# Performance work log

Hardware: AMD Instinct MI355X
Metric: run time of the kernel (lower is better)

The kernel has to match this reference:

```python
import jax, jax.numpy as jnp
import numpy as np

DIM = 1024
N_HEADS = 16
HEAD_DIM = DIM // N_HEADS


def setup_inputs() -> dict:
    key = jax.random.key(0)
    k_x, k_qkv, k_out = jax.random.split(key, 3)
    B, L = 4, 2048
    x = jax.random.normal(k_x, (B, L, DIM), dtype=jnp.float32)
    # torch Linear weight has shape [out, in]; y = x @ W.T
    s = 1.0 / np.sqrt(DIM)
    W_qkv = jax.random.uniform(k_qkv, (3 * DIM, DIM), dtype=jnp.float32, minval=-s, maxval=s)
    W_out = jax.random.uniform(k_out, (DIM, DIM), dtype=jnp.float32, minval=-s, maxval=s)
    return {"x": x, "W_qkv": W_qkv, "W_out": W_out}


def reference(x, W_qkv, W_out):
    B, L, D = x.shape
    H, Hd = N_HEADS, HEAD_DIM
    scale = Hd ** (-0.5)
    qkv = x @ W_qkv.T                       # [B, L, 3D]
    q, k, v = jnp.split(qkv, 3, axis=-1)
    # 'b l (h d) -> b h l d'
    q = q.reshape(B, L, H, Hd).transpose(0, 2, 1, 3)
    k = k.reshape(B, L, H, Hd).transpose(0, 2, 1, 3)
    v = v.reshape(B, L, H, Hd).transpose(0, 2, 1, 3)
    attn = jnp.einsum('bhld,bhmd->bhlm', q, k) * scale  # [B, H, L, L]
    causal = jnp.tril(jnp.ones((L, L), dtype=bool))
    attn = jnp.where(causal, attn, -jnp.inf)
    attn = jax.nn.softmax(attn, axis=-1)
    out = jnp.einsum('bhlm,bhmd->bhld', attn, v)        # [B, H, L, Hd]
    out = out.transpose(0, 2, 1, 3).reshape(B, L, D)    # 'b h l d -> b l (h d)'
    return out @ W_out.T
```

## Files before the change

kernel.cpp:

```cpp
#include <hip/hip_runtime.h>
#include <stdint.h>

#define BATCH 4
#define SEQ   2048
#define DIM_  1024
#define NHEAD 16
#define HDIM  64

#define QSC 0.18033688011112042f

typedef __attribute__((ext_vector_type(8)))  short bf8;
typedef __attribute__((ext_vector_type(4)))  short s4v;
typedef __attribute__((ext_vector_type(4)))  float f4;
typedef __attribute__((ext_vector_type(16))) float f16v;
typedef __attribute__((ext_vector_type(2)))  unsigned int u2;
typedef __attribute__((ext_vector_type(4)))  unsigned int u4;

#define MFMA(a, b, c)   __builtin_amdgcn_mfma_f32_16x16x32_bf16(a, b, c, 0, 0, 0)
#define MFMA32(a, b, c) __builtin_amdgcn_mfma_f32_32x32x16_bf16(a, b, c, 0, 0, 0)

#define BAR_LGKM() asm volatile("s_waitcnt lgkmcnt(0)\n\ts_barrier" ::: "memory")
#define PBAR() asm volatile("s_barrier" ::: "memory")

static __device__ __forceinline__ short f2b(float f) {
    uint32_t u = __builtin_bit_cast(uint32_t, f);
    u = (u + 0x7FFFu + ((u >> 16) & 1u)) >> 16;
    return (short)u;
}

static __device__ __forceinline__ uint32_t cvtpk(float lo, float hi) {
    uint32_t r;
    asm("v_cvt_pk_bf16_f32 %0, %1, %2" : "=v"(r) : "v"(lo), "v"(hi));
    return r;
}

typedef const uint32_t __attribute__((address_space(1)))* gas_t;
typedef uint32_t __attribute__((address_space(3)))* las_t;
static __device__ __forceinline__ void gl_lds16(const short* g, short* l) {
    __builtin_amdgcn_global_load_lds((gas_t)g, (las_t)l, 16, 0, 0);
}

__global__ void cvt_all(const float* __restrict__ x, const float* __restrict__ wq,
                        const float* __restrict__ wo, short* __restrict__ xb,
                        short* __restrict__ wqb, short* __restrict__ wob) {
    const int NX = BATCH * SEQ * DIM_ / 4, NQ = 3 * DIM_ * DIM_ / 4;
    int i = blockIdx.x * blockDim.x + threadIdx.x;
    const float4* in; s4v* out; int j;
    if (i < NX)           { in = (const float4*)x;  out = (s4v*)xb;  j = i; }
    else if (i < NX + NQ) { in = (const float4*)wq; out = (s4v*)wqb; j = i - NX; }
    else                  { in = (const float4*)wo; out = (s4v*)wob; j = i - NX - NQ; }
    float4 v = in[j];
    s4v o;
    o.x = f2b(v.x); o.y = f2b(v.y); o.z = f2b(v.z); o.w = f2b(v.w);
    out[j] = o;
}

#define LDSB 24576
#define NT   16

#define PG_PROLOG()                                                           \
    __shared__ __align__(16) short lds[3 * LDSB];                             \
    const int tid  = threadIdx.x;                                             \
    const int lane = tid & 63;                                                \
    const int wave = tid >> 6;                                                \
    const int quad = lane >> 4, l16 = lane & 15;                              \
    const int wr = wave >> 1, wc = wave & 1;                                  \
    const int m0 = blockIdx.y * 256;                                          \
    const int n0 = blockIdx.x * 128;                                          \
    \
    const short* gA[4]; int dA[4];                                            \
    _Pragma("unroll") for (int j = 0; j < 4; ++j) {                           \
        const int idx = j * 512 + tid;                                        \
        const int row = idx >> 3, pos = idx & 7;                              \
        gA[j] = A + (size_t)(m0 + row) * 1024 + (pos ^ (row & 7)) * 8;        \
        dA[j] = idx * 8;                                                      \
    }                                                                         \
    const short* gB[2]; int dB[2];                                            \
    _Pragma("unroll") for (int j = 0; j < 2; ++j) {                           \
        const int idx = j * 512 + tid;                                        \
        const int row = idx >> 3, pos = idx & 7;                              \
        gB[j] = W + (size_t)(n0 + row) * 1024 + (pos ^ (row & 7)) * 8;        \
        dB[j] = 16384 + idx * 8;                                              \
    }                                                                         \
                       \
    int aro[4], bro[4];                                                       \
    _Pragma("unroll") for (int i = 0; i < 4; ++i) {                           \
        aro[i] = (wr * 64 + i * 16 + l16) * 64;                               \
        bro[i] = 16384 + (wc * 64 + i * 16 + l16) * 64;                       \
    }                                                                         \
    const int kx = l16 & 7;                                                   \
    short* cur = lds; short* nxt = lds + LDSB; short* stg = lds + 2 * LDSB;   \
    f4 acc[4][4] = {};

#define PG_STAGE6(bp)                                                         \
    do {                                                                      \
        gl_lds16(gA[0], (bp) + dA[0]); gl_lds16(gA[1], (bp) + dA[1]);         \
        gl_lds16(gA[2], (bp) + dA[2]); gl_lds16(gA[3], (bp) + dA[3]);         \
        gl_lds16(gB[0], (bp) + dB[0]); gl_lds16(gB[1], (bp) + dB[1]);         \
        _Pragma("unroll") for (int j = 0; j < 4; ++j) gA[j] += 64;            \
        gB[0] += 64; gB[1] += 64;                                             \
    } while (0)

#define PG_KLOOP()                                                            \
    PG_STAGE6(cur);                                               \
    PG_STAGE6(nxt);                                               \
    asm volatile("s_waitcnt vmcnt(6)\n\ts_barrier" ::: "memory");             \
    for (int t = 0; t < NT; ++t) {                                            \
        const bool pre = (t < NT - 2);                                        \
        bf8 a[4], b[4];                                                       \
                                              \
        _Pragma("unroll") for (int i = 0; i < 4; ++i) {                       \
            a[i] = *(const bf8*)(cur + aro[i] + ((0 + quad) ^ kx) * 8);       \
            b[i] = *(const bf8*)(cur + bro[i] + ((0 + quad) ^ kx) * 8);       \
        }                                                                     \
        if (pre) {                                                            \
            gl_lds16(gA[0], stg + dA[0]); gl_lds16(gA[1], stg + dA[1]);       \
            gl_lds16(gA[2], stg + dA[2]);                                     \
        }                                                                     \
        PBAR();                                                               \
        __builtin_amdgcn_s_setprio(1);                                        \
        _Pragma("unroll") for (int mt = 0; mt < 4; ++mt)                      \
            _Pragma("unroll") for (int nt = 0; nt < 4; ++nt)                  \
                acc[mt][nt] = MFMA(a[mt], b[nt], acc[mt][nt]);                \
        __builtin_amdgcn_s_setprio(0);                                        \
        PBAR();                                                               \
                                              \
        _Pragma("unroll") for (int i = 0; i < 4; ++i) {                       \
            a[i] = *(const bf8*)(cur + aro[i] + ((4 + quad) ^ kx) * 8);       \
            b[i] = *(const bf8*)(cur + bro[i] + ((4 + quad) ^ kx) * 8);       \
        }                                                                     \
        if (pre) {                                                            \
            gl_lds16(gA[3], stg + dA[3]);                                     \
            gl_lds16(gB[0], stg + dB[0]); gl_lds16(gB[1], stg + dB[1]);       \
            _Pragma("unroll") for (int j = 0; j < 4; ++j) gA[j] += 64;        \
            gB[0] += 64; gB[1] += 64;                                         \
        }                                                                     \
        PBAR();                                                               \
        __builtin_amdgcn_s_setprio(1);                                        \
        _Pragma("unroll") for (int mt = 0; mt < 4; ++mt)                      \
            _Pragma("unroll") for (int nt = 0; nt < 4; ++nt)                  \
                acc[mt][nt] = MFMA(a[mt], b[nt], acc[mt][nt]);                \
        __builtin_amdgcn_s_setprio(0);                                        \
         \
        if (pre) asm volatile("s_waitcnt vmcnt(6)\n\ts_barrier" ::: "memory");\
        else     asm volatile("s_waitcnt vmcnt(0)\n\ts_barrier" ::: "memory");\
        short* tmp = cur; cur = nxt; nxt = stg; stg = tmp;                    \
    }

__global__ __launch_bounds__(512, 2) void gemm_qkv(const short* __restrict__ A,
                                                   const short* __restrict__ W,
                                                   short* __restrict__ Qd,
                                                   short* __restrict__ Kd,
                                                   short* __restrict__ Vd) {
    PG_PROLOG();
    PG_KLOOP();

    short* const bases[3] = {Qd, Kd, Vd};
    #pragma unroll
    for (int mt = 0; mt < 4; ++mt) {
        const int row = m0 + wr * 64 + mt * 16 + quad * 4;
        #pragma unroll
        for (int nt = 0; nt < 4; ++nt) {
            const int colb  = n0 + wc * 64 + nt * 16;
            const int which = colb >> 10;
            const int hh    = (colb >> 6) & 15;
            const int d0    = colb & 63;
            const float sc_ = (which == 0) ? QSC : 1.0f;
            short* bp = bases[which];
            #pragma unroll
            for (int r = 0; r < 4; ++r) {
                const int t  = row + r;
                const int bb = t >> 11, ll = t & 2047;
                bp[((size_t)(bb * NHEAD + hh) * SEQ + ll) * 64 + d0 + l16] =
                    f2b(acc[mt][nt][r] * sc_);
            }
        }
    }
}

__global__ __launch_bounds__(512, 2) void gemm_bt(const short* __restrict__ A,
                                                  const short* __restrict__ W,
                                                  float* __restrict__ Cp) {
    PG_PROLOG();
    PG_KLOOP();

    #pragma unroll
    for (int mt = 0; mt < 4; ++mt) {
        const int row = m0 + wr * 64 + mt * 16 + quad * 4;
        #pragma unroll
        for (int nt = 0; nt < 4; ++nt) {
            const int col = n0 + wc * 64 + nt * 16 + l16;
            #pragma unroll
            for (int r = 0; r < 4; ++r)
                Cp[(size_t)(row + r) * DIM_ + col] = acc[mt][nt][r];
        }
    }
}

__global__ __launch_bounds__(256) void flash_attn(const short* __restrict__ Qd,
                                                  const short* __restrict__ Kd,
                                                  const short* __restrict__ Vd,
                                                  short* __restrict__ out) {
    const int bh = blockIdx.x;
    const int b  = bh >> 4, h = bh & 15;
    const int qt = (gridDim.y - 1) - blockIdx.y;
    const int q0 = qt * 128;
    const int tid  = threadIdx.x;
    const int lane = tid & 63, wave = tid >> 6;
    const int l32  = lane & 31, khalf = lane >> 5;

    __shared__ __align__(16) short Ks[64 * 72];
    __shared__ __align__(16) short Vt[64 * 72];
    uint32_t* Vt32 = (uint32_t*)Vt;

    const short* Qp = Qd + (size_t)bh * (SEQ * 64);
    const short* Kp = Kd + (size_t)bh * (SEQ * 64);
    const short* Vp = Vd + (size_t)bh * (SEQ * 64);

    const int qrow = q0 + wave * 32 + l32;
    bf8 qf[4];
    #pragma unroll
    for (int dk = 0; dk < 4; ++dk)
        qf[dk] = *(const bf8*)(Qp + (size_t)qrow * 64 + dk * 16 + khalf * 8);

    const int skey = tid >> 2, sc = tid & 3;
    const int vkp = tid & 31, vds = (tid >> 5) * 8;

    bf8 ka0 = *(const bf8*)(Kp + (size_t)skey * 64 + sc * 8);
    bf8 ka1 = *(const bf8*)(Kp + (size_t)skey * 64 + (sc + 4) * 8);
    bf8 vr0 = *(const bf8*)(Vp + (size_t)(2 * vkp) * 64 + vds);
    bf8 vr1 = *(const bf8*)(Vp + (size_t)(2 * vkp + 1) * 64 + vds);

    f16v o0 = {}, o1 = {};
    float lsum = 0.f;
    const bf8 zz = {};

    const int nIter = 2 * qt + 2;
    for (int it = 0; it < nIter; ++it) {
        const int k0 = it * 64;

        BAR_LGKM();
        *(bf8*)(&Ks[skey * 72 + sc * 8])       = ka0;
        *(bf8*)(&Ks[skey * 72 + (sc + 4) * 8]) = ka1;
        #pragma unroll
        for (int i = 0; i < 8; ++i) {
            uint32_t p = (uint32_t)(uint16_t)vr0[i] | ((uint32_t)(uint16_t)vr1[i] << 16);
            Vt32[(vds + i) * 36 + vkp] = p;
        }
        BAR_LGKM();

        if (it + 1 < nIter) {
            const int kn = k0 + 64;
            ka0 = *(const bf8*)(Kp + (size_t)(kn + skey) * 64 + sc * 8);
            ka1 = *(const bf8*)(Kp + (size_t)(kn + skey) * 64 + (sc + 4) * 8);
            vr0 = *(const bf8*)(Vp + (size_t)(kn + 2 * vkp) * 64 + vds);
            vr1 = *(const bf8*)(Vp + (size_t)(kn + 2 * vkp + 1) * 64 + vds);
        }

        if (q0 + wave * 32 < k0) continue;

        bf8 pf[4];
        #pragma unroll
        for (int kt = 0; kt < 2; ++kt) {
            const int ktbase = k0 + kt * 32;
            const int rel = (q0 + wave * 32) - ktbase;
            if (rel < 0) {
                pf[kt * 2] = zz; pf[kt * 2 + 1] = zz;
                continue;
            }
            f16v st = {};
            __builtin_amdgcn_s_setprio(1);
            #pragma unroll
            for (int dk = 0; dk < 4; ++dk) {
                bf8 kf = *(const bf8*)(&Ks[(kt * 32 + l32) * 72 + dk * 16 + khalf * 8]);
                st = MFMA32(kf, qf[dk], st);
            }
            __builtin_amdgcn_s_setprio(0);
            float P[16];
            if (rel == 0) {
                #pragma unroll
                for (int r = 0; r < 16; ++r) {
                    const int kg = ktbase + (r & 3) + 8 * (r >> 2) + 4 * khalf;
                    float pv = __builtin_amdgcn_exp2f(st[r]);
                    P[r] = (kg > qrow) ? 0.0f : pv;
                }
            } else {
                #pragma unroll
                for (int r = 0; r < 16; ++r) P[r] = __builtin_amdgcn_exp2f(st[r]);
            }
            uint32_t w0 = cvtpk(P[0],  P[1]),  w1 = cvtpk(P[2],  P[3]);
            uint32_t w2 = cvtpk(P[4],  P[5]),  w3 = cvtpk(P[6],  P[7]);
            uint32_t w4 = cvtpk(P[8],  P[9]),  w5 = cvtpk(P[10], P[11]);
            uint32_t w6 = cvtpk(P[12], P[13]), w7 = cvtpk(P[14], P[15]);
            u2 s02 = __builtin_amdgcn_permlane32_swap(w0, w2, false, false);
            u2 s13 = __builtin_amdgcn_permlane32_swap(w1, w3, false, false);
            u2 s46 = __builtin_amdgcn_permlane32_swap(w4, w6, false, false);
            u2 s57 = __builtin_amdgcn_permlane32_swap(w5, w7, false, false);
            u4 q0w = {s02[0], s13[0], s02[1], s13[1]};
            u4 q1w = {s46[0], s57[0], s46[1], s57[1]};
            pf[kt * 2]     = __builtin_bit_cast(bf8, q0w);
            pf[kt * 2 + 1] = __builtin_bit_cast(bf8, q1w);
            float ls = ((P[0] + P[1]) + (P[2] + P[3])) +
                       ((P[4] + P[5]) + (P[6] + P[7])) +
                       ((P[8] + P[9]) + (P[10] + P[11])) +
                       ((P[12] + P[13]) + (P[14] + P[15]));
            lsum += ls;
        }

        __builtin_amdgcn_s_setprio(1);
        #pragma unroll
        for (int ks = 0; ks < 4; ++ks) {
            bf8 v0 = *(const bf8*)(&Vt[(l32) * 72 + ks * 16 + khalf * 8]);
            bf8 v1 = *(const bf8*)(&Vt[(32 + l32) * 72 + ks * 16 + khalf * 8]);
            o0 = MFMA32(pf[ks], v0, o0);
            o1 = MFMA32(pf[ks], v1, o1);
        }
        __builtin_amdgcn_s_setprio(0);
    }

    lsum += __shfl_xor(lsum, 32);
    short* outp = out + ((size_t)(b * SEQ + q0 + wave * 32) * DIM_) + h * 64;
    #pragma unroll
    for (int r = 0; r < 16; ++r) {
        const int rowl = (r & 3) + 8 * (r >> 2) + 4 * khalf;
        const float inv = 1.0f / __shfl(lsum, rowl);
        outp[(size_t)rowl * DIM_ + l32]      = f2b(o0[r] * inv);
        outp[(size_t)rowl * DIM_ + 32 + l32] = f2b(o1[r] * inv);
    }
}

extern "C" void kernel_launch(void* const* d_in, const int* in_sizes, int n_in,
                              void* d_out, int out_size, void* d_ws, size_t ws_size,
                              hipStream_t stream) {
    const float* x    = (const float*)d_in[0];
    const float* wqkv = (const float*)d_in[1];
    const float* wout = (const float*)d_in[2];

    char* ws = (char*)d_ws;
    short* xb    = (short*)(ws);
    short* wqkvb = (short*)(ws + (size_t)(16) * (1 << 20));
    short* woutb = (short*)(ws + (size_t)(22) * (1 << 20));
    short* Qd    = (short*)(ws + (size_t)(24) * (1 << 20));
    short* Kd    = (short*)(ws + (size_t)(40) * (1 << 20));
    short* Vd    = (short*)(ws + (size_t)(56) * (1 << 20));
    short* attnb = (short*)(ws + (size_t)(72) * (1 << 20));

    const int ntot = (BATCH * SEQ * DIM_ + 3 * DIM_ * DIM_ + DIM_ * DIM_) / 4;
    cvt_all<<<(ntot + 255) / 256, 256, 0, stream>>>(x, wqkv, wout, xb, wqkvb, woutb);

    gemm_qkv<<<dim3(3 * DIM_ / 128, BATCH * SEQ / 256), 512, 0, stream>>>(
        xb, wqkvb, Qd, Kd, Vd);

    flash_attn<<<dim3(BATCH * NHEAD, SEQ / 128), 256, 0, stream>>>(Qd, Kd, Vd, attnb);

    gemm_bt<<<dim3(DIM_ / 128, BATCH * SEQ / 256), 512, 0, stream>>>(
        attnb, woutb, (float*)d_out);
}
```

Baseline: 232.4 us.

## Enlarge GEMM tiles to 256x256 with double-buffered LDS and swizzled block order

Both projection GEMMs move from 256x128 tiles with triple-buffered LDS to 256x256 tiles with two LDS buffers. Each wave now computes a 128x64 sub-tile, and the k-loop is split into four MFMA phases with finer-grained global-to-LDS prefetch and waits. Workgroup IDs are remapped by a modular swizzle to improve L2 reuse across neighbouring blocks. The larger tile raises arithmetic intensity but doubles accumulator registers (128 floats per thread) and halves grid size (384 and 128 blocks), which can cost occupancy or leave CUs idle on the output GEMM.

Measured after the change: 235.8 us. About the same (+1.5%).

```diff
diff --git a/kernel.cpp b/kernel.cpp
--- a/kernel.cpp
+++ b/kernel.cpp
@@ -55,96 +55,101 @@
     out[j] = o;
 }
 
-#define LDSB 24576
-#define NT   16
+#define NT 16
 
 #define PG_PROLOG()                                                           \
-    __shared__ __align__(16) short lds[3 * LDSB];                             \
+    __shared__ __align__(16) short lds[2 * 32768];                            \
     const int tid  = threadIdx.x;                                             \
     const int lane = tid & 63;                                                \
     const int wave = tid >> 6;                                                \
     const int quad = lane >> 4, l16 = lane & 15;                              \
-    const int wr = wave >> 1, wc = wave & 1;                                  \
-    const int m0 = blockIdx.y * 256;                                          \
-    const int n0 = blockIdx.x * 128;                                          \
-    \
-    const short* gA[4]; int dA[4];                                            \
+    const int wr = wave >> 2, wc = wave & 3;                                  \
+                     \
+    const int gx  = gridDim.x;                                                \
+    const int nwg = gx * gridDim.y;                                           \
+    const int lid = blockIdx.y * gx + blockIdx.x;                             \
+    const int swz = (lid & 7) * (nwg >> 3) + (lid >> 3);                      \
+    const int m0 = (swz / gx) * 256;                                          \
+    const int n0 = (swz % gx) * 256;                                          \
+    const short* gA[4]; const short* gB[4]; int dA[4];                        \
     _Pragma("unroll") for (int j = 0; j < 4; ++j) {                           \
         const int idx = j * 512 + tid;                                        \
         const int row = idx >> 3, pos = idx & 7;                              \
         gA[j] = A + (size_t)(m0 + row) * 1024 + (pos ^ (row & 7)) * 8;        \
+        gB[j] = W + (size_t)(n0 + row) * 1024 + (pos ^ (row & 7)) * 8;        \
         dA[j] = idx * 8;                                                      \
     }                                                                         \
-    const short* gB[2]; int dB[2];                                            \
-    _Pragma("unroll") for (int j = 0; j < 2; ++j) {                           \
-        const int idx = j * 512 + tid;                                        \
-        const int row = idx >> 3, pos = idx & 7;                              \
-        gB[j] = W + (size_t)(n0 + row) * 1024 + (pos ^ (row & 7)) * 8;        \
-        dB[j] = 16384 + idx * 8;                                              \
-    }                                                                         \
-                       \
-    int aro[4], bro[4];                                                       \
-    _Pragma("unroll") for (int i = 0; i < 4; ++i) {                           \
-        aro[i] = (wr * 64 + i * 16 + l16) * 64;                               \
-        bro[i] = 16384 + (wc * 64 + i * 16 + l16) * 64;                       \
-    }                                                                         \
-    const int kx = l16 & 7;                                                   \
-    short* cur = lds; short* nxt = lds + LDSB; short* stg = lds + 2 * LDSB;   \
-    f4 acc[4][4] = {};
-
-#define PG_STAGE6(bp)                                                         \
-    do {                                                                      \
-        gl_lds16(gA[0], (bp) + dA[0]); gl_lds16(gA[1], (bp) + dA[1]);         \
-        gl_lds16(gA[2], (bp) + dA[2]); gl_lds16(gA[3], (bp) + dA[3]);         \
-        gl_lds16(gB[0], (bp) + dB[0]); gl_lds16(gB[1], (bp) + dB[1]);         \
-        _Pragma("unroll") for (int j = 0; j < 4; ++j) gA[j] += 64;            \
-        gB[0] += 64; gB[1] += 64;                                             \
-    } while (0)
+    int aoff[8], boff[4];                                                     \
+    _Pragma("unroll") for (int i = 0; i < 8; ++i)                             \
+        aoff[i] = (wr * 128 + i * 16 + l16) * 64;                             \
+    _Pragma("unroll") for (int i = 0; i < 4; ++i)                             \
+        boff[i] = 16384 + (wc * 64 + i * 16 + l16) * 64;                      \
+    const int kx  = l16 & 7;                                                  \
+    const int kc0 = ((0 + quad) ^ kx) * 8;                                    \
+    const int kc1 = ((4 + quad) ^ kx) * 8;                                    \
+    short* cur = lds; short* nxt = lds + 32768;                               \
+    f4 acc[8][4] = {};
+
+#define PG_ISSUE_B01(bp) do { gl_lds16(gB[0], (bp) + 16384 + dA[0]);          \
+                              gl_lds16(gB[1], (bp) + 16384 + dA[1]); } while (0)
+#define PG_ISSUE_B23(bp) do { gl_lds16(gB[2], (bp) + 16384 + dA[2]);          \
+                              gl_lds16(gB[3], (bp) + 16384 + dA[3]); } while (0)
+#define PG_ISSUE_A(bp)   do { gl_lds16(gA[0], (bp) + dA[0]);                  \
+                              gl_lds16(gA[2], (bp) + dA[2]);                  \
+                              gl_lds16(gA[1], (bp) + dA[1]);                  \
+                              gl_lds16(gA[3], (bp) + dA[3]); } while (0)
+#define PG_BUMP() _Pragma("unroll") for (int j = 0; j < 4; ++j) { gA[j] += 64; gB[j] += 64; }
+
+#define PG_MFMA16(ACCB, AV)                                                   \
+    __builtin_amdgcn_s_setprio(1);                                            \
+    _Pragma("unroll") for (int mt = 0; mt < 4; ++mt)                          \
+        _Pragma("unroll") for (int nt = 0; nt < 4; ++nt)                      \
+            acc[ACCB + mt][nt] = MFMA(AV[mt], b[nt], acc[ACCB + mt][nt]);     \
+    __builtin_amdgcn_s_setprio(0);
 
 #define PG_KLOOP()                                                            \
-    PG_STAGE6(cur);                                               \
-    PG_STAGE6(nxt);                                               \
-    asm volatile("s_waitcnt vmcnt(6)\n\ts_barrier" ::: "memory");             \
+    PG_ISSUE_B01(cur); PG_ISSUE_B23(cur); PG_ISSUE_A(cur);                    \
+    PG_BUMP();                                                                \
+    asm volatile("s_waitcnt vmcnt(2)\n\ts_barrier" ::: "memory");             \
     for (int t = 0; t < NT; ++t) {                                            \
-        const bool pre = (t < NT - 2);                                        \
+        const bool pre = (t < NT - 1);                                        \
         bf8 a[4], b[4];                                                       \
-                                              \
+                                                \
         _Pragma("unroll") for (int i = 0; i < 4; ++i) {                       \
-            a[i] = *(const bf8*)(cur + aro[i] + ((0 + quad) ^ kx) * 8);       \
-            b[i] = *(const bf8*)(cur + bro[i] + ((0 + quad) ^ kx) * 8);       \
+            a[i] = *(const bf8*)(cur + aoff[i] + kc0);                        \
+            b[i] = *(const bf8*)(cur + boff[i] + kc0);                        \
         }                                                                     \
-        if (pre) {                                                            \
-            gl_lds16(gA[0], stg + dA[0]); gl_lds16(gA[1], stg + dA[1]);       \
-            gl_lds16(gA[2], stg + dA[2]);                                     \
+        if (pre) PG_ISSUE_B01(nxt);                                           \
+        PBAR();                                                               \
+        PG_MFMA16(0, a);                                                      \
+                     \
+        if (pre) asm volatile("s_waitcnt vmcnt(2)\n\ts_barrier" ::: "memory");\
+        else     asm volatile("s_waitcnt vmcnt(0)\n\ts_barrier" ::: "memory");\
+                                     \
+        bf8 a2[4];                                                            \
+        _Pragma("unroll") for (int i = 0; i < 4; ++i)                         \
+            a2[i] = *(const bf8*)(cur + aoff[4 + i] + kc0);                   \
+        if (pre) PG_ISSUE_B23(nxt);                                           \
+        PBAR();                                                               \
+        PG_MFMA16(4, a2);                                                     \
+        PBAR();                                                               \
+                                                \
+        _Pragma("unroll") for (int i = 0; i < 4; ++i) {                       \
+            a[i] = *(const bf8*)(cur + aoff[i] + kc1);                        \
+            b[i] = *(const bf8*)(cur + boff[i] + kc1);                        \
         }                                                                     \
-        PBAR();                                                               \
-        __builtin_amdgcn_s_setprio(1);                                        \
-        _Pragma("unroll") for (int mt = 0; mt < 4; ++mt)                      \
-            _Pragma("unroll") for (int nt = 0; nt < 4; ++nt)                  \
-                acc[mt][nt] = MFMA(a[mt], b[nt], acc[mt][nt]);                \
-        __builtin_amdgcn_s_setprio(0);                                        \
-        PBAR();                                                               \
-                                              \
-        _Pragma("unroll") for (int i = 0; i < 4; ++i) {                       \
-            a[i] = *(const bf8*)(cur + aro[i] + ((4 + quad) ^ kx) * 8);       \
-            b[i] = *(const bf8*)(cur + bro[i] + ((4 + quad) ^ kx) * 8);       \
-        }                                                                     \
-        if (pre) {                                                            \
-            gl_lds16(gA[3], stg + dA[3]);                                     \
-            gl_lds16(gB[0], stg + dB[0]); gl_lds16(gB[1], stg + dB[1]);       \
-            _Pragma("unroll") for (int j = 0; j < 4; ++j) gA[j] += 64;        \
-            gB[0] += 64; gB[1] += 64;                                         \
-        }                                                                     \
-        PBAR();                                                               \
-        __builtin_amdgcn_s_setprio(1);                                        \
-        _Pragma("unroll") for (int mt = 0; mt < 4; ++mt)                      \
-            _Pragma("unroll") for (int nt = 0; nt < 4; ++nt)                  \
-                acc[mt][nt] = MFMA(a[mt], b[nt], acc[mt][nt]);                \
-        __builtin_amdgcn_s_setprio(0);                                        \
-         \
-        if (pre) asm volatile("s_waitcnt vmcnt(6)\n\ts_barrier" ::: "memory");\
-        else     asm volatile("s_waitcnt vmcnt(0)\n\ts_barrier" ::: "memory");\
-        short* tmp = cur; cur = nxt; nxt = stg; stg = tmp;                    \
+        if (pre) { PG_ISSUE_A(nxt); PG_BUMP(); }                              \
+        PBAR();                                                               \
+        PG_MFMA16(0, a);                                                      \
+        PBAR();                                                               \
+                                                \
+        _Pragma("unroll") for (int i = 0; i < 4; ++i)                         \
+            a2[i] = *(const bf8*)(cur + aoff[4 + i] + kc1);                   \
+        PBAR();                                                               \
+        PG_MFMA16(4, a2);                                                     \
+               \
+        if (pre) asm volatile("s_waitcnt vmcnt(2)\n\ts_barrier" ::: "memory");\
+        short* tmp = cur; cur = nxt; nxt = tmp;                               \
     }
 
 __global__ __launch_bounds__(512, 2) void gemm_qkv(const short* __restrict__ A,
@@ -157,11 +162,11 @@
 
     short* const bases[3] = {Qd, Kd, Vd};
     #pragma unroll
-    for (int mt = 0; mt < 4; ++mt) {
-        const int row = m0 + wr * 64 + mt * 16 + quad * 4;
-        #pragma unroll
-        for (int nt = 0; nt < 4; ++nt) {
-            const int colb  = n0 + wc * 64 + nt * 16;
+    for (int mf = 0; mf < 8; ++mf) {
+        const int row = m0 + wr * 128 + mf * 16 + quad * 4;
+        #pragma unroll
+        for (int nf = 0; nf < 4; ++nf) {
+            const int colb  = n0 + wc * 64 + nf * 16;
             const int which = colb >> 10;
             const int hh    = (colb >> 6) & 15;
             const int d0    = colb & 63;
@@ -169,10 +174,10 @@
             short* bp = bases[which];
             #pragma unroll
             for (int r = 0; r < 4; ++r) {
-                const int t  = row + r;
-                const int bb = t >> 11, ll = t & 2047;
+                const int tk = row + r;
+                const int bb = tk >> 11, ll = tk & 2047;
                 bp[((size_t)(bb * NHEAD + hh) * SEQ + ll) * 64 + d0 + l16] =
-                    f2b(acc[mt][nt][r] * sc_);
+                    f2b(acc[mf][nf][r] * sc_);
             }
         }
     }
@@ -185,14 +190,14 @@
     PG_KLOOP();
 
     #pragma unroll
-    for (int mt = 0; mt < 4; ++mt) {
-        const int row = m0 + wr * 64 + mt * 16 + quad * 4;
-        #pragma unroll
-        for (int nt = 0; nt < 4; ++nt) {
-            const int col = n0 + wc * 64 + nt * 16 + l16;
+    for (int mf = 0; mf < 8; ++mf) {
+        const int row = m0 + wr * 128 + mf * 16 + quad * 4;
+        #pragma unroll
+        for (int nf = 0; nf < 4; ++nf) {
+            const int col = n0 + wc * 64 + nf * 16 + l16;
             #pragma unroll
             for (int r = 0; r < 4; ++r)
-                Cp[(size_t)(row + r) * DIM_ + col] = acc[mt][nt][r];
+                Cp[(size_t)(row + r) * DIM_ + col] = acc[mf][nf][r];
         }
     }
 }
@@ -348,11 +353,11 @@
     const int ntot = (BATCH * SEQ * DIM_ + 3 * DIM_ * DIM_ + DIM_ * DIM_) / 4;
     cvt_all<<<(ntot + 255) / 256, 256, 0, stream>>>(x, wqkv, wout, xb, wqkvb, woutb);
 
-    gemm_qkv<<<dim3(3 * DIM_ / 128, BATCH * SEQ / 256), 512, 0, stream>>>(
+    gemm_qkv<<<dim3(3 * DIM_ / 256, BATCH * SEQ / 256), 512, 0, stream>>>(
         xb, wqkvb, Qd, Kd, Vd);
 
     flash_attn<<<dim3(BATCH * NHEAD, SEQ / 128), 256, 0, stream>>>(Qd, Kd, Vd, attnb);
 
-    gemm_bt<<<dim3(DIM_ / 128, BATCH * SEQ / 256), 512, 0, stream>>>(
+    gemm_bt<<<dim3(DIM_ / 256, BATCH * SEQ / 256), 512, 0, stream>>>(
         attnb, woutb, (float*)d_out);
 }
```

## Pair causal query tiles per block, double-buffer K/V LDS, swizzle GEMM block order

Applied to the files above, without the earlier changes.

The flash-attention grid is halved so each block handles two query tiles, one long (15-y) and one short (y). This evens out the causal workload per block and removes the tail imbalance. K/V LDS tiles are now double-buffered, alternating by iteration parity. The GEMM prologue remaps block IDs with an XCD-style swizzle (lid&7 spread) so neighbouring tiles share L2. The risks are fewer blocks for occupancy, extra LDS per block, and a serial second tile that could lengthen per-block latency.

New measurement: 248.3 us. +6.9%, slower.

```diff
diff --git a/kernel.cpp b/kernel.cpp
--- a/kernel.cpp
+++ b/kernel.cpp
@@ -20,7 +20,6 @@
 #define MFMA32(a, b, c) __builtin_amdgcn_mfma_f32_32x32x16_bf16(a, b, c, 0, 0, 0)
 
 #define BAR_LGKM() asm volatile("s_waitcnt lgkmcnt(0)\n\ts_barrier" ::: "memory")
-#define PBAR() asm volatile("s_barrier" ::: "memory")
 
 static __device__ __forceinline__ short f2b(float f) {
     uint32_t u = __builtin_bit_cast(uint32_t, f);
@@ -58,6 +57,8 @@
 #define LDSB 24576
 #define NT   16
 
+#define PBAR() asm volatile("s_barrier" ::: "memory")
+
 #define PG_PROLOG()                                                           \
     __shared__ __align__(16) short lds[3 * LDSB];                             \
     const int tid  = threadIdx.x;                                             \
@@ -65,8 +66,12 @@
     const int wave = tid >> 6;                                                \
     const int quad = lane >> 4, l16 = lane & 15;                              \
     const int wr = wave >> 1, wc = wave & 1;                                  \
-    const int m0 = blockIdx.y * 256;                                          \
-    const int n0 = blockIdx.x * 128;                                          \
+    const int gx  = gridDim.x;                                                \
+    const int nwg = gx * gridDim.y;                                           \
+    const int lid = blockIdx.y * gx + blockIdx.x;                             \
+    const int swz = (lid & 7) * (nwg >> 3) + (lid >> 3);                      \
+    const int m0 = (swz / gx) * 256;                                          \
+    const int n0 = (swz % gx) * 128;                                          \
     \
     const short* gA[4]; int dA[4];                                            \
     _Pragma("unroll") for (int j = 0; j < 4; ++j) {                           \
@@ -203,129 +208,139 @@
                                                   short* __restrict__ out) {
     const int bh = blockIdx.x;
     const int b  = bh >> 4, h = bh & 15;
-    const int qt = (gridDim.y - 1) - blockIdx.y;
-    const int q0 = qt * 128;
     const int tid  = threadIdx.x;
     const int lane = tid & 63, wave = tid >> 6;
     const int l32  = lane & 31, khalf = lane >> 5;
 
-    __shared__ __align__(16) short Ks[64 * 72];
-    __shared__ __align__(16) short Vt[64 * 72];
-    uint32_t* Vt32 = (uint32_t*)Vt;
+    __shared__ __align__(16) short Ks[2][64 * 72];
+    __shared__ __align__(16) short Vt[2][64 * 72];
 
     const short* Qp = Qd + (size_t)bh * (SEQ * 64);
     const short* Kp = Kd + (size_t)bh * (SEQ * 64);
     const short* Vp = Vd + (size_t)bh * (SEQ * 64);
 
-    const int qrow = q0 + wave * 32 + l32;
-    bf8 qf[4];
-    #pragma unroll
-    for (int dk = 0; dk < 4; ++dk)
-        qf[dk] = *(const bf8*)(Qp + (size_t)qrow * 64 + dk * 16 + khalf * 8);
-
     const int skey = tid >> 2, sc = tid & 3;
     const int vkp = tid & 31, vds = (tid >> 5) * 8;
 
-    bf8 ka0 = *(const bf8*)(Kp + (size_t)skey * 64 + sc * 8);
-    bf8 ka1 = *(const bf8*)(Kp + (size_t)skey * 64 + (sc + 4) * 8);
-    bf8 vr0 = *(const bf8*)(Vp + (size_t)(2 * vkp) * 64 + vds);
-    bf8 vr1 = *(const bf8*)(Vp + (size_t)(2 * vkp + 1) * 64 + vds);
-
-    f16v o0 = {}, o1 = {};
-    float lsum = 0.f;
     const bf8 zz = {};
 
-    const int nIter = 2 * qt + 2;
-    for (int it = 0; it < nIter; ++it) {
-        const int k0 = it * 64;
-
-        BAR_LGKM();
-        *(bf8*)(&Ks[skey * 72 + sc * 8])       = ka0;
-        *(bf8*)(&Ks[skey * 72 + (sc + 4) * 8]) = ka1;
+    #pragma unroll 1
+    for (int half = 0; half < 2; ++half) {
+        const int qt = half ? blockIdx.y : (15 - blockIdx.y);
+        const int q0 = qt * 128;
+
+        const int qrow = q0 + wave * 32 + l32;
+        bf8 qf[4];
         #pragma unroll
-        for (int i = 0; i < 8; ++i) {
-            uint32_t p = (uint32_t)(uint16_t)vr0[i] | ((uint32_t)(uint16_t)vr1[i] << 16);
-            Vt32[(vds + i) * 36 + vkp] = p;
+        for (int dk = 0; dk < 4; ++dk)
+            qf[dk] = *(const bf8*)(Qp + (size_t)qrow * 64 + dk * 16 + khalf * 8);
+
+        bf8 ka0 = *(const bf8*)(Kp + (size_t)skey * 64 + sc * 8);
+        bf8 ka1 = *(const bf8*)(Kp + (size_t)skey * 64 + (sc + 4) * 8);
+        bf8 vr0 = *(const bf8*)(Vp + (size_t)(2 * vkp) * 64 + vds);
+        bf8 vr1 = *(const bf8*)(Vp + (size_t)(2 * vkp + 1) * 64 + vds);
+
+        f16v o0 = {}, o1 = {};
+        float lsum = 0.f;
+
+        const int nIter = 2 * qt + 2;
+        for (int it = 0; it < nIter; ++it) {
+            const int k0 = it * 64;
+            const int pb = it & 1;
+            short* Kb = Ks[pb];
+            short* Vb = Vt[pb];
+            uint32_t* Vb32 = (uint32_t*)Vb;
+
+            BAR_LGKM();
+            *(bf8*)(&Kb[skey * 72 + sc * 8])       = ka0;
+            *(bf8*)(&Kb[skey * 72 + (sc + 4) * 8]) = ka1;
+            #pragma unroll
+            for (int i = 0; i < 8; ++i) {
+                uint32_t p = (uint32_t)(uint16_t)vr0[i] |
+                             ((uint32_t)(uint16_t)vr1[i] << 16);
+                Vb32[(vds + i) * 36 + vkp] = p;
+            }
+            BAR_LGKM();
+
+            if (it + 1 < nIter) {
+                const int kn = k0 + 64;
+                ka0 = *(const bf8*)(Kp + (size_t)(kn + skey) * 64 + sc * 8);
+                ka1 = *(const bf8*)(Kp + (size_t)(kn + skey) * 64 + (sc + 4) * 8);
+                vr0 = *(const bf8*)(Vp + (size_t)(kn + 2 * vkp) * 64 + vds);
+                vr1 = *(const bf8*)(Vp + (size_t)(kn + 2 * vkp + 1) * 64 + vds);
+            }
+
+            if (q0 + wave * 32 < k0) continue;
+
+            bf8 pf[4];
+            #pragma unroll
+            for (int kt = 0; kt < 2; ++kt) {
+                const int ktbase = k0 + kt * 32;
+                const int rel = (q0 + wave * 32) - ktbase;
+                if (rel < 0) {
+                    pf[kt * 2] = zz; pf[kt * 2 + 1] = zz;
+                    continue;
+                }
+                f16v st = {};
+                __builtin_amdgcn_s_setprio(1);
+                #pragma unroll
+                for (int dk = 0; dk < 4; ++dk) {
+                    bf8 kf = *(const bf8*)(&Kb[(kt * 32 + l32) * 72 +
+                                               dk * 16 + khalf * 8]);
+                    st = MFMA32(kf, qf[dk], st);
+                }
+                __builtin_amdgcn_s_setprio(0);
+                float P[16];
+                if (rel == 0) {
+                    #pragma unroll
+                    for (int r = 0; r < 16; ++r) {
+                        const int kg = ktbase + (r & 3) + 8 * (r >> 2) + 4 * khalf;
+                        float pv = __builtin_amdgcn_exp2f(st[r]);
+                        P[r] = (kg > qrow) ? 0.0f : pv;
+                    }
+                } else {
+                    #pragma unroll
+                    for (int r = 0; r < 16; ++r) P[r] = __builtin_amdgcn_exp2f(st[r]);
+                }
+                uint32_t w0 = cvtpk(P[0],  P[1]),  w1 = cvtpk(P[2],  P[3]);
+                uint32_t w2 = cvtpk(P[4],  P[5]),  w3 = cvtpk(P[6],  P[7]);
+                uint32_t w4 = cvtpk(P[8],  P[9]),  w5 = cvtpk(P[10], P[11]);
+                uint32_t w6 = cvtpk(P[12], P[13]), w7 = cvtpk(P[14], P[15]);
+                u2 s02 = __builtin_amdgcn_permlane32_swap(w0, w2, false, false);
+                u2 s13 = __builtin_amdgcn_permlane32_swap(w1, w3, false, false);
+                u2 s46 = __builtin_amdgcn_permlane32_swap(w4, w6, false, false);
+                u2 s57 = __builtin_amdgcn_permlane32_swap(w5, w7, false, false);
+                u4 q0w = {s02[0], s13[0], s02[1], s13[1]};
+                u4 q1w = {s46[0], s57[0], s46[1], s57[1]};
+                pf[kt * 2]     = __builtin_bit_cast(bf8, q0w);
+                pf[kt * 2 + 1] = __builtin_bit_cast(bf8, q1w);
+                float ls = ((P[0] + P[1]) + (P[2] + P[3])) +
+                           ((P[4] + P[5]) + (P[6] + P[7])) +
+                           ((P[8] + P[9]) + (P[10] + P[11])) +
+                           ((P[12] + P[13]) + (P[14] + P[15]));
+                lsum += ls;
+            }
+
+            __builtin_amdgcn_s_setprio(1);
+            #pragma unroll
+            for (int ks = 0; ks < 4; ++ks) {
+                bf8 v0 = *(const bf8*)(&Vb[(l32) * 72 + ks * 16 + khalf * 8]);
+                bf8 v1 = *(const bf8*)(&Vb[(32 + l32) * 72 + ks * 16 + khalf * 8]);
+                o0 = MFMA32(pf[ks], v0, o0);
+                o1 = MFMA32(pf[ks], v1, o1);
+            }
+            __builtin_amdgcn_s_setprio(0);
         }
-        BAR_LGKM();
-
-        if (it + 1 < nIter) {
-            const int kn = k0 + 64;
-            ka0 = *(const bf8*)(Kp + (size_t)(kn + skey) * 64 + sc * 8);
-            ka1 = *(const bf8*)(Kp + (size_t)(kn + skey) * 64 + (sc + 4) * 8);
-            vr0 = *(const bf8*)(Vp + (size_t)(kn + 2 * vkp) * 64 + vds);
-            vr1 = *(const bf8*)(Vp + (size_t)(kn + 2 * vkp + 1) * 64 + vds);
+
+        lsum += __shfl_xor(lsum, 32);
+        short* outp = out + ((size_t)(b * SEQ + q0 + wave * 32) * DIM_) + h * 64;
+        #pragma unroll
+        for (int r = 0; r < 16; ++r) {
+            const int rowl = (r & 3) + 8 * (r >> 2) + 4 * khalf;
+            const float inv = 1.0f / __shfl(lsum, rowl);
+            outp[(size_t)rowl * DIM_ + l32]      = f2b(o0[r] * inv);
+            outp[(size_t)rowl * DIM_ + 32 + l32] = f2b(o1[r] * inv);
         }
-
-        if (q0 + wave * 32 < k0) continue;
-
-        bf8 pf[4];
-        #pragma unroll
-        for (int kt = 0; kt < 2; ++kt) {
-            const int ktbase = k0 + kt * 32;
-            const int rel = (q0 + wave * 32) - ktbase;
-            if (rel < 0) {
-                pf[kt * 2] = zz; pf[kt * 2 + 1] = zz;
-                continue;
-            }
-            f16v st = {};
-            __builtin_amdgcn_s_setprio(1);
-            #pragma unroll
-            for (int dk = 0; dk < 4; ++dk) {
-                bf8 kf = *(const bf8*)(&Ks[(kt * 32 + l32) * 72 + dk * 16 + khalf * 8]);
-                st = MFMA32(kf, qf[dk], st);
-            }
-            __builtin_amdgcn_s_setprio(0);
-            float P[16];
-            if (rel == 0) {
-                #pragma unroll
-                for (int r = 0; r < 16; ++r) {
-                    const int kg = ktbase + (r & 3) + 8 * (r >> 2) + 4 * khalf;
-                    float pv = __builtin_amdgcn_exp2f(st[r]);
-                    P[r] = (kg > qrow) ? 0.0f : pv;
-                }
-            } else {
-                #pragma unroll
-                for (int r = 0; r < 16; ++r) P[r] = __builtin_amdgcn_exp2f(st[r]);
-            }
-            uint32_t w0 = cvtpk(P[0],  P[1]),  w1 = cvtpk(P[2],  P[3]);
-            uint32_t w2 = cvtpk(P[4],  P[5]),  w3 = cvtpk(P[6],  P[7]);
-            uint32_t w4 = cvtpk(P[8],  P[9]),  w5 = cvtpk(P[10], P[11]);
-            uint32_t w6 = cvtpk(P[12], P[13]), w7 = cvtpk(P[14], P[15]);
-            u2 s02 = __builtin_amdgcn_permlane32_swap(w0, w2, false, false);
-            u2 s13 = __builtin_amdgcn_permlane32_swap(w1, w3, false, false);
-            u2 s46 = __builtin_amdgcn_permlane32_swap(w4, w6, false, false);
-            u2 s57 = __builtin_amdgcn_permlane32_swap(w5, w7, false, false);
-            u4 q0w = {s02[0], s13[0], s02[1], s13[1]};
-            u4 q1w = {s46[0], s57[0], s46[1], s57[1]};
-            pf[kt * 2]     = __builtin_bit_cast(bf8, q0w);
-            pf[kt * 2 + 1] = __builtin_bit_cast(bf8, q1w);
-            float ls = ((P[0] + P[1]) + (P[2] + P[3])) +
-                       ((P[4] + P[5]) + (P[6] + P[7])) +
-                       ((P[8] + P[9]) + (P[10] + P[11])) +
-                       ((P[12] + P[13]) + (P[14] + P[15]));
-            lsum += ls;
-        }
-
-        __builtin_amdgcn_s_setprio(1);
-        #pragma unroll
-        for (int ks = 0; ks < 4; ++ks) {
-            bf8 v0 = *(const bf8*)(&Vt[(l32) * 72 + ks * 16 + khalf * 8]);
-            bf8 v1 = *(const bf8*)(&Vt[(32 + l32) * 72 + ks * 16 + khalf * 8]);
-            o0 = MFMA32(pf[ks], v0, o0);
-            o1 = MFMA32(pf[ks], v1, o1);
-        }
-        __builtin_amdgcn_s_setprio(0);
-    }
-
-    lsum += __shfl_xor(lsum, 32);
-    short* outp = out + ((size_t)(b * SEQ + q0 + wave * 32) * DIM_) + h * 64;
-    #pragma unroll
-    for (int r = 0; r < 16; ++r) {
-        const int rowl = (r & 3) + 8 * (r >> 2) + 4 * khalf;
-        const float inv = 1.0f / __shfl(lsum, rowl);
-        outp[(size_t)rowl * DIM_ + l32]      = f2b(o0[r] * inv);
-        outp[(size_t)rowl * DIM_ + 32 + l32] = f2b(o1[r] * inv);
     }
 }
 
@@ -351,7 +366,7 @@
     gemm_qkv<<<dim3(3 * DIM_ / 128, BATCH * SEQ / 256), 512, 0, stream>>>(
         xb, wqkvb, Qd, Kd, Vd);
 
-    flash_attn<<<dim3(BATCH * NHEAD, SEQ / 128), 256, 0, stream>>>(Qd, Kd, Vd, attnb);
+    flash_attn<<<dim3(BATCH * NHEAD, 8), 256, 0, stream>>>(Qd, Kd, Vd, attnb);
 
     gemm_bt<<<dim3(DIM_ / 128, BATCH * SEQ / 256), 512, 0, stream>>>(
         attnb, woutb, (float*)d_out);
```
